# Optimization experiments

Measured on AMD Instinct MI355X. Metric: run time of the kernel, lower is better.

Reference implementation:

```python
import jax, jax.numpy as jnp
import numpy as np

D_MODEL = 1024
N_HEADS = 16
D_K = D_MODEL // N_HEADS


def setup_inputs() -> dict:
    key = jax.random.key(0)
    kx, kq, kk, kv, ko = jax.random.split(key, 5)
    s = 1.0 / np.sqrt(D_MODEL)
    return {
        "x": jax.random.normal(kx, (4, 2048, D_MODEL), dtype=jnp.float32),
        "W_q": jax.random.normal(kq, (D_MODEL, D_MODEL), dtype=jnp.float32) * s,
        "W_k": jax.random.normal(kk, (D_MODEL, D_MODEL), dtype=jnp.float32) * s,
        "W_v": jax.random.normal(kv, (D_MODEL, D_MODEL), dtype=jnp.float32) * s,
        "W_o": jax.random.normal(ko, (D_MODEL, D_MODEL), dtype=jnp.float32) * s,
    }


def reference(x, W_q, W_k, W_v, W_o):
    B, S, _ = x.shape
    # torch nn.Linear computes x @ W.T; our W_* stored as [out, in]-equivalent square,
    # use plain x @ W (equivalent parameterization for a random weight).
    def split_heads(t):  # [B,S,D] -> [B,H,S,d_k]
        return t.reshape(B, S, N_HEADS, D_K).transpose(0, 2, 1, 3)

    Q = split_heads(x @ W_q)
    K = split_heads(x @ W_k)
    V = split_heads(x @ W_v)
    scale = 1.0 / np.sqrt(D_K).astype(np.float32)
    scores = jnp.einsum('bhqd,bhkd->bhqk', Q, K) * scale  # [B,H,S,S]
    causal_mask = jnp.tril(jnp.ones((S, S), dtype=bool))  # True = keep
    scores = jnp.where(causal_mask, scores, jnp.float32(-jnp.inf))
    attn = jax.nn.softmax(scores, axis=-1)
    out = jnp.einsum('bhqk,bhkd->bhqd', attn, V)  # [B,H,S,d_k]
    out = out.transpose(0, 2, 1, 3).reshape(B, S, D_MODEL)
    return out @ W_o
```

## Files before the change

kernel.cpp:

```cpp
#include <hip/hip_runtime.h>
#include <hip/hip_bf16.h>
#include <stdint.h>

#define B_SZ 4
#define SEQ 2048
#define DM 1024
#define NH 16
#define DK 64
#define BH (B_SZ * NH)
#define M_TOT (B_SZ * SEQ)

typedef unsigned short u16;
typedef u16 u16x8 __attribute__((ext_vector_type(8)));
typedef __bf16 bf16x8 __attribute__((ext_vector_type(8)));
typedef float f32x4 __attribute__((ext_vector_type(4)));

__device__ __forceinline__ u16 f2bf(float f) {
    union { float f; uint32_t u; } v; v.f = f;
    uint32_t u = v.u;
    return (u16)((u + 0x7FFFu + ((u >> 16) & 1u)) >> 16);
}

__device__ __forceinline__ u16 f2bf_trunc(float f) {
    union { float f; uint32_t u; } v; v.f = f;
    return (u16)(v.u >> 16);
}

__device__ __forceinline__ f32x4 mfma16(u16x8 a, u16x8 b, f32x4 c) {
    return __builtin_amdgcn_mfma_f32_16x16x32_bf16(
        __builtin_bit_cast(bf16x8, a), __builtin_bit_cast(bf16x8, b), c, 0, 0, 0);
}

__device__ __forceinline__ void gload16_lds(const void* g, void* l) {
    __builtin_amdgcn_global_load_lds(
        (const __attribute__((address_space(1))) void*)(uintptr_t)g,
        (__attribute__((address_space(3))) void*)(uintptr_t)l, 16, 0, 0);
}

__global__ void cvt_bf16_kernel(const float* __restrict__ in, u16* __restrict__ out, int n4) {
    int i = blockIdx.x * blockDim.x + threadIdx.x;
    if (i < n4) {
        float4 v = ((const float4*)in)[i];
        ushort4 o;
        o.x = f2bf(v.x); o.y = f2bf(v.y); o.z = f2bf(v.z); o.w = f2bf(v.w);
        ((ushort4*)out)[i] = o;
    }
}

__global__ void transpose_w_kernel(const float* __restrict__ W0, const float* __restrict__ W1,
                                   u16* __restrict__ Wt) {
    __shared__ u16 tile[32][33];
    int bx = blockIdx.x, by = blockIdx.y, z = blockIdx.z;
    const float* W = z ? W1 : W0;
    u16* Wd = Wt + (size_t)z * DM * DM;
    int t = threadIdx.x;
    for (int i = 0; i < 4; i++) {
        int idx = t + i * 256;
        int r = idx >> 5, c = idx & 31;
        tile[r][c] = f2bf(W[(by * 32 + r) * DM + bx * 32 + c]);
    }
    __syncthreads();
    for (int i = 0; i < 4; i++) {
        int idx = t + i * 256;
        int r2 = idx >> 5, c2 = idx & 31;
        Wd[(bx * 32 + r2) * DM + by * 32 + c2] = tile[c2][r2];
    }
}

template <int AFP32, int MODE>
__global__ __launch_bounds__(256, 2) void gemm128(
    const void* __restrict__ Ain, const u16* __restrict__ Bt,
    void* __restrict__ C0p, void* __restrict__ C1p, float scale0) {
    __shared__ u16 As[128][32];
    __shared__ u16 Bs[128][32];
    const int K = DM;
    int m0 = blockIdx.x * 128;
    int n0 = blockIdx.y * 128;
    int tid = threadIdx.x;
    int lane = tid & 63, wave = tid >> 6;
    int quad = lane >> 4, l15 = lane & 15;
    int wm = wave >> 1, wn = wave & 1;

    f32x4 acc[4][4];
    for (int i = 0; i < 4; i++)
        for (int j = 0; j < 4; j++) acc[i][j] = f32x4{0.f, 0.f, 0.f, 0.f};

    int rS = lane >> 2;
    int cS = (lane & 3) * 8;

    for (int k0 = 0; k0 < K; k0 += 32) {
        __syncthreads();
        if (AFP32) {
            const float* A = (const float*)Ain;
            for (int i = 0; i < 4; i++) {
                int idx = tid + i * 256;
                int r = idx >> 3, c = (idx & 7) * 4;
                float4 v = *(const float4*)(&A[(size_t)(m0 + r) * K + k0 + c]);
                ushort4 o;
                o.x = f2bf(v.x); o.y = f2bf(v.y); o.z = f2bf(v.z); o.w = f2bf(v.w);
                *(ushort4*)(&As[r][c]) = o;
            }
        } else {
            const u16* A = (const u16*)Ain;
            const u16* ga = &A[(size_t)(m0 + wave * 32 + rS) * K + k0 + cS];
            gload16_lds(ga, &As[wave * 32][0]);
            gload16_lds(ga + (size_t)16 * K, &As[wave * 32 + 16][0]);
        }
        {
            const u16* gb = &Bt[(size_t)(n0 + wave * 32 + rS) * K + k0 + cS];
            gload16_lds(gb, &Bs[wave * 32][0]);
            gload16_lds(gb + (size_t)16 * K, &Bs[wave * 32 + 16][0]);
        }
        __syncthreads();
        u16x8 af[4], bfv[4];
        for (int mt = 0; mt < 4; mt++)
            af[mt] = *(const u16x8*)(&As[wm * 64 + mt * 16 + l15][quad * 8]);
        for (int nt = 0; nt < 4; nt++)
            bfv[nt] = *(const u16x8*)(&Bs[wn * 64 + nt * 16 + l15][quad * 8]);
        for (int mt = 0; mt < 4; mt++)
            for (int nt = 0; nt < 4; nt++)
                acc[mt][nt] = mfma16(af[mt], bfv[nt], acc[mt][nt]);
    }

    for (int mt = 0; mt < 4; mt++)
        for (int nt = 0; nt < 4; nt++)
            for (int r = 0; r < 4; r++) {
                int m = m0 + wm * 64 + mt * 16 + quad * 4 + r;
                int n = n0 + wn * 64 + nt * 16 + l15;
                float v = acc[mt][nt][r];
                if (MODE == 0) {
                    v *= (n < 1024) ? scale0 : 1.0f;
                    u16* C = (n < 1024) ? (u16*)C0p : (u16*)C1p;
                    int ne = n & 1023;
                    int b = m >> 11, s = m & 2047;
                    int h = ne >> 6, d = ne & 63;
                    C[(((size_t)(b * NH + h) * SEQ) + s) * DK + d] = f2bf(v);
                } else if (MODE == 1) {
                    ((float*)C0p)[(size_t)m * DM + n] = v;
                } else {
                    int b = m >> 11, s = m & 2047;
                    int h = n >> 6, d = n & 63;
                    ((u16*)C0p)[(((size_t)(b * NH + h) * DK) + d) * SEQ + s] = f2bf(v);
                }
            }
}

__global__ __launch_bounds__(256, 6) void attn_kernel(
    const u16* __restrict__ Qb, const u16* __restrict__ Kb,
    const u16* __restrict__ Vtb, u16* __restrict__ AOb) {
    __shared__ u16 Kl[2][64][32];
    __shared__ u16 Vl[2][64][32];
    __shared__ u16 Pl[64][68];

    int bh = blockIdx.x;
    int qs = 31 - blockIdx.y;
    int q0 = qs * 64;
    int tid = threadIdx.x, lane = tid & 63, wave = tid >> 6;
    int quad = lane >> 4, l15 = lane & 15;
    int b = bh >> 4, h = bh & 15;

    const u16* Qg = Qb + (size_t)bh * SEQ * DK;
    const u16* Kg = Kb + (size_t)bh * SEQ * DK;
    const u16* Vg = Vtb + (size_t)bh * DK * SEQ;

    int rS = lane >> 2;
    int cS = (lane & 3) * 8;
    u16* Pw = &Pl[wave * 16][0];

    u16x8 aq[2];
    for (int kc = 0; kc < 2; kc++)
        aq[kc] = *(const u16x8*)(
            &Qg[(size_t)(q0 + wave * 16 + l15) * DK + kc * 32 + quad * 8]);

    float lsum[4];
    f32x4 O[4];
    for (int r = 0; r < 4; r++) lsum[r] = 0.f;
    for (int nt = 0; nt < 4; nt++) O[nt] = f32x4{0.f, 0.f, 0.f, 0.f};

    for (int kt = 0; kt <= qs; kt++) {
        int k0 = kt * 64;
        __syncthreads();
        {
            const u16* gk = &Kg[(size_t)(k0 + wave * 16 + rS) * DK + cS];
            gload16_lds(gk, &Kl[0][wave * 16][0]);
            gload16_lds(gk + 32, &Kl[1][wave * 16][0]);
            const u16* gv = &Vg[(size_t)(wave * 16 + rS) * SEQ + k0 + cS];
            gload16_lds(gv, &Vl[0][wave * 16][0]);
            gload16_lds(gv + 32, &Vl[1][wave * 16][0]);
        }
        __syncthreads();

        f32x4 sc[4];
        for (int nt = 0; nt < 4; nt++) {
            u16x8 b0 = *(const u16x8*)(&Kl[0][nt * 16 + l15][quad * 8]);
            u16x8 b1 = *(const u16x8*)(&Kl[1][nt * 16 + l15][quad * 8]);
            f32x4 z = f32x4{0.f, 0.f, 0.f, 0.f};
            z = mfma16(aq[0], b0, z);
            z = mfma16(aq[1], b1, z);
            sc[nt] = z;
        }
        if (kt == qs) {
            for (int nt = 0; nt < 4; nt++)
                for (int r = 0; r < 4; r++) {
                    int qq = wave * 16 + quad * 4 + r;
                    int kk = nt * 16 + l15;
                    float e = exp2f(sc[nt][r]);
                    float pv = (kk <= qq) ? e : 0.f;
                    sc[nt][r] = pv;
                    lsum[r] += pv;
                }
        } else {
            for (int nt = 0; nt < 4; nt++)
                for (int r = 0; r < 4; r++) {
                    float pv = exp2f(sc[nt][r]);
                    sc[nt][r] = pv;
                    lsum[r] += pv;
                }
        }
        for (int nt = 0; nt < 4; nt++)
            for (int r = 0; r < 4; r++)
                Pw[(size_t)(quad * 4 + r) * 68 + nt * 16 + l15] = f2bf_trunc(sc[nt][r]);
        u16x8 ap0 = *(const u16x8*)(&Pw[(size_t)l15 * 68 + quad * 8]);
        u16x8 ap1 = *(const u16x8*)(&Pw[(size_t)l15 * 68 + 32 + quad * 8]);
        for (int nt = 0; nt < 4; nt++) {
            u16x8 b0 = *(const u16x8*)(&Vl[0][nt * 16 + l15][quad * 8]);
            u16x8 b1 = *(const u16x8*)(&Vl[1][nt * 16 + l15][quad * 8]);
            O[nt] = mfma16(ap0, b0, O[nt]);
            O[nt] = mfma16(ap1, b1, O[nt]);
        }
    }

    for (int r = 0; r < 4; r++) {
        float s = lsum[r];
        for (int off = 1; off < 16; off <<= 1) s += __shfl_xor(s, off, 64);
        float inv = 1.0f / s;
        int q = q0 + wave * 16 + quad * 4 + r;
        for (int nt = 0; nt < 4; nt++) {
            int d = nt * 16 + l15;
            AOb[((size_t)(b * SEQ + q)) * DM + h * DK + d] = f2bf(O[nt][r] * inv);
        }
    }
}

extern "C" void kernel_launch(void* const* d_in, const int* in_sizes, int n_in,
                              void* d_out, int out_size, void* d_ws, size_t ws_size,
                              hipStream_t stream) {
    const float* x = (const float*)d_in[0];
    const float* Wq = (const float*)d_in[1];
    const float* Wk = (const float*)d_in[2];
    const float* Wv = (const float*)d_in[3];
    const float* Wo = (const float*)d_in[4];
    float* out = (float*)d_out;

    const size_t HALF = (size_t)M_TOT * DM * 2;
    char* S0 = (char*)d_ws;
    char* S1 = (char*)d_ws + HALF;
    char* D0 = (char*)d_out;
    char* D1 = (char*)d_out + HALF;

    u16* xb  = (u16*)S0;
    u16* Qb  = (u16*)S1;
    u16* Kb  = (u16*)D1;
    u16* Vt  = (u16*)D0;
    u16* AOb = (u16*)S0;
    u16* wqk = (u16*)D0;
    u16* wvt = (u16*)S0;
    u16* wot = (u16*)S1;

    const float cscale = 0.125f * 1.44269504088896f;
    dim3 tg2(32, 32, 2);
    dim3 tg1(32, 32, 1);
    dim3 gg(M_TOT / 128, DM / 128);

    int n4 = M_TOT * DM / 4;
    cvt_bf16_kernel<<<n4 / 256, 256, 0, stream>>>(x, xb, n4);

    transpose_w_kernel<<<tg2, 256, 0, stream>>>(Wq, Wk, wqk);
    dim3 gqk(M_TOT / 128, 2048 / 128);
    gemm128<0, 0><<<gqk, 256, 0, stream>>>(xb, wqk, (void*)Qb, (void*)Kb, cscale);

    transpose_w_kernel<<<tg1, 256, 0, stream>>>(Wv, Wv, wvt);
    gemm128<1, 2><<<gg, 256, 0, stream>>>(x, wvt, (void*)Vt, (void*)Vt, 1.0f);

    dim3 ag(BH, 32);
    attn_kernel<<<ag, 256, 0, stream>>>(Qb, Kb, Vt, AOb);

    transpose_w_kernel<<<tg1, 256, 0, stream>>>(Wo, Wo, wot);
    gemm128<0, 1><<<gg, 256, 0, stream>>>(AOb, wot, (void*)out, (void*)out, 1.0f);
}
```

Measured before the change: 296.6 us.

## Restructure attention to per-wave paired query strips and widen GEMM K-tile

```diff
diff --git a/kernel.cpp b/kernel.cpp
--- a/kernel.cpp
+++ b/kernel.cpp
@@ -71,8 +71,8 @@
 __global__ __launch_bounds__(256, 2) void gemm128(
     const void* __restrict__ Ain, const u16* __restrict__ Bt,
     void* __restrict__ C0p, void* __restrict__ C1p, float scale0) {
-    __shared__ u16 As[128][32];
-    __shared__ u16 Bs[128][32];
+    __shared__ u16 As[128][64];
+    __shared__ u16 Bs[128][64];
     const int K = DM;
     int m0 = blockIdx.x * 128;
     int n0 = blockIdx.y * 128;
@@ -85,41 +85,47 @@
     for (int i = 0; i < 4; i++)
         for (int j = 0; j < 4; j++) acc[i][j] = f32x4{0.f, 0.f, 0.f, 0.f};
 
-    int rS = lane >> 2;
-    int cS = (lane & 3) * 8;
-
-    for (int k0 = 0; k0 < K; k0 += 32) {
+    int r8 = lane >> 3;
+    int c8 = (lane & 7) * 8;
+
+    for (int k0 = 0; k0 < K; k0 += 64) {
         __syncthreads();
         if (AFP32) {
             const float* A = (const float*)Ain;
-            for (int i = 0; i < 4; i++) {
-                int idx = tid + i * 256;
-                int r = idx >> 3, c = (idx & 7) * 4;
-                float4 v = *(const float4*)(&A[(size_t)(m0 + r) * K + k0 + c]);
-                ushort4 o;
-                o.x = f2bf(v.x); o.y = f2bf(v.y); o.z = f2bf(v.z); o.w = f2bf(v.w);
-                *(ushort4*)(&As[r][c]) = o;
+            for (int j = 0; j < 4; j++) {
+                int slot = tid + j * 256;
+                int r = slot >> 3, c = (slot & 7) * 8;
+                const float* g = &A[(size_t)(m0 + r) * K + k0 + c];
+                float4 v0 = *(const float4*)g;
+                float4 v1 = *(const float4*)(g + 4);
+                u16x8 o;
+                o[0] = f2bf(v0.x); o[1] = f2bf(v0.y); o[2] = f2bf(v0.z); o[3] = f2bf(v0.w);
+                o[4] = f2bf(v1.x); o[5] = f2bf(v1.y); o[6] = f2bf(v1.z); o[7] = f2bf(v1.w);
+                *(u16x8*)(&As[r][c]) = o;
             }
         } else {
             const u16* A = (const u16*)Ain;
-            const u16* ga = &A[(size_t)(m0 + wave * 32 + rS) * K + k0 + cS];
-            gload16_lds(ga, &As[wave * 32][0]);
-            gload16_lds(ga + (size_t)16 * K, &As[wave * 32 + 16][0]);
+            const u16* ga = &A[(size_t)(m0 + wave * 32 + r8) * K + k0 + c8];
+            for (int j = 0; j < 4; j++)
+                gload16_lds(ga + (size_t)(8 * j) * K, &As[wave * 32 + 8 * j][0]);
         }
         {
-            const u16* gb = &Bt[(size_t)(n0 + wave * 32 + rS) * K + k0 + cS];
-            gload16_lds(gb, &Bs[wave * 32][0]);
-            gload16_lds(gb + (size_t)16 * K, &Bs[wave * 32 + 16][0]);
+            const u16* gb = &Bt[(size_t)(n0 + wave * 32 + r8) * K + k0 + c8];
+            for (int j = 0; j < 4; j++)
+                gload16_lds(gb + (size_t)(8 * j) * K, &Bs[wave * 32 + 8 * j][0]);
         }
         __syncthreads();
-        u16x8 af[4], bfv[4];
+        u16x8 af[4][2], bfv[4][2];
         for (int mt = 0; mt < 4; mt++)
-            af[mt] = *(const u16x8*)(&As[wm * 64 + mt * 16 + l15][quad * 8]);
+            for (int kc = 0; kc < 2; kc++)
+                af[mt][kc] = *(const u16x8*)(&As[wm * 64 + mt * 16 + l15][kc * 32 + quad * 8]);
         for (int nt = 0; nt < 4; nt++)
-            bfv[nt] = *(const u16x8*)(&Bs[wn * 64 + nt * 16 + l15][quad * 8]);
-        for (int mt = 0; mt < 4; mt++)
-            for (int nt = 0; nt < 4; nt++)
-                acc[mt][nt] = mfma16(af[mt], bfv[nt], acc[mt][nt]);
+            for (int kc = 0; kc < 2; kc++)
+                bfv[nt][kc] = *(const u16x8*)(&Bs[wn * 64 + nt * 16 + l15][kc * 32 + quad * 8]);
+        for (int kc = 0; kc < 2; kc++)
+            for (int mt = 0; mt < 4; mt++)
+                for (int nt = 0; nt < 4; nt++)
+                    acc[mt][nt] = mfma16(af[mt][kc], bfv[nt][kc], acc[mt][nt]);
     }
 
     for (int mt = 0; mt < 4; mt++)
@@ -145,16 +151,13 @@
             }
 }
 
-__global__ __launch_bounds__(256, 6) void attn_kernel(
+__global__ __launch_bounds__(256, 4) void attn_kernel(
     const u16* __restrict__ Qb, const u16* __restrict__ Kb,
     const u16* __restrict__ Vtb, u16* __restrict__ AOb) {
-    __shared__ u16 Kl[2][64][32];
-    __shared__ u16 Vl[2][64][32];
-    __shared__ u16 Pl[64][68];
+    __shared__ u16 Pl[4][32][68];
 
     int bh = blockIdx.x;
-    int qs = 31 - blockIdx.y;
-    int q0 = qs * 64;
+    int yy = blockIdx.y;
     int tid = threadIdx.x, lane = tid & 63, wave = tid >> 6;
     int quad = lane >> 4, l15 = lane & 15;
     int b = bh >> 4, h = bh & 15;
@@ -162,83 +165,92 @@
     const u16* Qg = Qb + (size_t)bh * SEQ * DK;
     const u16* Kg = Kb + (size_t)bh * SEQ * DK;
     const u16* Vg = Vtb + (size_t)bh * DK * SEQ;
-
-    int rS = lane >> 2;
-    int cS = (lane & 3) * 8;
-    u16* Pw = &Pl[wave * 16][0];
-
-    u16x8 aq[2];
-    for (int kc = 0; kc < 2; kc++)
-        aq[kc] = *(const u16x8*)(
-            &Qg[(size_t)(q0 + wave * 16 + l15) * DK + kc * 32 + quad * 8]);
-
-    float lsum[4];
-    f32x4 O[4];
-    for (int r = 0; r < 4; r++) lsum[r] = 0.f;
-    for (int nt = 0; nt < 4; nt++) O[nt] = f32x4{0.f, 0.f, 0.f, 0.f};
-
-    for (int kt = 0; kt <= qs; kt++) {
-        int k0 = kt * 64;
-        __syncthreads();
-        {
-            const u16* gk = &Kg[(size_t)(k0 + wave * 16 + rS) * DK + cS];
-            gload16_lds(gk, &Kl[0][wave * 16][0]);
-            gload16_lds(gk + 32, &Kl[1][wave * 16][0]);
-            const u16* gv = &Vg[(size_t)(wave * 16 + rS) * SEQ + k0 + cS];
-            gload16_lds(gv, &Vl[0][wave * 16][0]);
-            gload16_lds(gv + 32, &Vl[1][wave * 16][0]);
-        }
-        __syncthreads();
-
-        f32x4 sc[4];
-        for (int nt = 0; nt < 4; nt++) {
-            u16x8 b0 = *(const u16x8*)(&Kl[0][nt * 16 + l15][quad * 8]);
-            u16x8 b1 = *(const u16x8*)(&Kl[1][nt * 16 + l15][quad * 8]);
-            f32x4 z = f32x4{0.f, 0.f, 0.f, 0.f};
-            z = mfma16(aq[0], b0, z);
-            z = mfma16(aq[1], b1, z);
-            sc[nt] = z;
-        }
-        if (kt == qs) {
+    u16* Pw = &Pl[wave][0][0];
+
+    for (int ph = 0; ph < 2; ph++) {
+        int s0 = yy * 4 + wave;
+        int strip = ph ? (63 - s0) : s0;
+        int q0 = strip * 32;
+        int lastkt = strip >> 1;
+
+        u16x8 aq[2][2];
+        for (int m = 0; m < 2; m++)
+            for (int kc = 0; kc < 2; kc++)
+                aq[m][kc] = *(const u16x8*)(
+                    &Qg[(size_t)(q0 + m * 16 + l15) * DK + kc * 32 + quad * 8]);
+
+        float lsum[2][4];
+        f32x4 O[2][4];
+        for (int m = 0; m < 2; m++)
+            for (int r = 0; r < 4; r++) lsum[m][r] = 0.f;
+        for (int m = 0; m < 2; m++)
+            for (int nt = 0; nt < 4; nt++) O[m][nt] = f32x4{0.f, 0.f, 0.f, 0.f};
+
+        for (int kt = 0; kt <= lastkt; kt++) {
+            int k0 = kt * 64;
+            bool masked = (kt == lastkt);
+
+            u16x8 kf[4][2];
             for (int nt = 0; nt < 4; nt++)
-                for (int r = 0; r < 4; r++) {
-                    int qq = wave * 16 + quad * 4 + r;
-                    int kk = nt * 16 + l15;
-                    float e = exp2f(sc[nt][r]);
-                    float pv = (kk <= qq) ? e : 0.f;
-                    sc[nt][r] = pv;
-                    lsum[r] += pv;
+                for (int kc = 0; kc < 2; kc++)
+                    kf[nt][kc] = *(const u16x8*)(
+                        &Kg[(size_t)(k0 + nt * 16 + l15) * DK + kc * 32 + quad * 8]);
+
+            for (int nt = 0; nt < 4; nt++) {
+                for (int m = 0; m < 2; m++) {
+                    f32x4 z = f32x4{0.f, 0.f, 0.f, 0.f};
+                    z = mfma16(aq[m][0], kf[nt][0], z);
+                    z = mfma16(aq[m][1], kf[nt][1], z);
+                    if (masked) {
+                        for (int r = 0; r < 4; r++) {
+                            int qa = q0 + m * 16 + quad * 4 + r;
+                            int ka = k0 + nt * 16 + l15;
+                            float pv = (ka <= qa) ? exp2f(z[r]) : 0.f;
+                            lsum[m][r] += pv;
+                            Pw[(size_t)(m * 16 + quad * 4 + r) * 68 + nt * 16 + l15] =
+                                f2bf_trunc(pv);
+                        }
+                    } else {
+                        for (int r = 0; r < 4; r++) {
+                            float pv = exp2f(z[r]);
+                            lsum[m][r] += pv;
+                            Pw[(size_t)(m * 16 + quad * 4 + r) * 68 + nt * 16 + l15] =
+                                f2bf_trunc(pv);
+                        }
+                    }
                 }
-        } else {
+            }
+
+            u16x8 vf[4][2];
             for (int nt = 0; nt < 4; nt++)
-                for (int r = 0; r < 4; r++) {
-                    float pv = exp2f(sc[nt][r]);
-                    sc[nt][r] = pv;
-                    lsum[r] += pv;
+                for (int kc = 0; kc < 2; kc++)
+                    vf[nt][kc] = *(const u16x8*)(
+                        &Vg[(size_t)(nt * 16 + l15) * SEQ + k0 + kc * 32 + quad * 8]);
+
+            u16x8 ap[2][2];
+            for (int m = 0; m < 2; m++)
+                for (int kc = 0; kc < 2; kc++)
+                    ap[m][kc] = *(const u16x8*)(
+                        &Pw[(size_t)(m * 16 + l15) * 68 + kc * 32 + quad * 8]);
+
+            for (int nt = 0; nt < 4; nt++)
+                for (int m = 0; m < 2; m++) {
+                    O[m][nt] = mfma16(ap[m][0], vf[nt][0], O[m][nt]);
+                    O[m][nt] = mfma16(ap[m][1], vf[nt][1], O[m][nt]);
                 }
         }
-        for (int nt = 0; nt < 4; nt++)
-            for (int r = 0; r < 4; r++)
-                Pw[(size_t)(quad * 4 + r) * 68 + nt * 16 + l15] = f2bf_trunc(sc[nt][r]);
-        u16x8 ap0 = *(const u16x8*)(&Pw[(size_t)l15 * 68 + quad * 8]);
-        u16x8 ap1 = *(const u16x8*)(&Pw[(size_t)l15 * 68 + 32 + quad * 8]);
-        for (int nt = 0; nt < 4; nt++) {
-            u16x8 b0 = *(const u16x8*)(&Vl[0][nt * 16 + l15][quad * 8]);
-            u16x8 b1 = *(const u16x8*)(&Vl[1][nt * 16 + l15][quad * 8]);
-            O[nt] = mfma16(ap0, b0, O[nt]);
-            O[nt] = mfma16(ap1, b1, O[nt]);
-        }
-    }
-
-    for (int r = 0; r < 4; r++) {
-        float s = lsum[r];
-        for (int off = 1; off < 16; off <<= 1) s += __shfl_xor(s, off, 64);
-        float inv = 1.0f / s;
-        int q = q0 + wave * 16 + quad * 4 + r;
-        for (int nt = 0; nt < 4; nt++) {
-            int d = nt * 16 + l15;
-            AOb[((size_t)(b * SEQ + q)) * DM + h * DK + d] = f2bf(O[nt][r] * inv);
-        }
+
+        for (int m = 0; m < 2; m++)
+            for (int r = 0; r < 4; r++) {
+                float s = lsum[m][r];
+                for (int off = 1; off < 16; off <<= 1) s += __shfl_xor(s, off, 64);
+                float inv = 1.0f / s;
+                int q = q0 + m * 16 + quad * 4 + r;
+                for (int nt = 0; nt < 4; nt++) {
+                    int d = nt * 16 + l15;
+                    AOb[((size_t)(b * SEQ + q)) * DM + h * DK + d] = f2bf(O[m][nt][r] * inv);
+                }
+            }
     }
 }
 
@@ -282,7 +294,7 @@
     transpose_w_kernel<<<tg1, 256, 0, stream>>>(Wv, Wv, wvt);
     gemm128<1, 2><<<gg, 256, 0, stream>>>(x, wvt, (void*)Vt, (void*)Vt, 1.0f);
 
-    dim3 ag(BH, 32);
+    dim3 ag(BH, 16);
     attn_kernel<<<ag, 256, 0, stream>>>(Qb, Kb, Vt, AOb);
 
     transpose_w_kernel<<<tg1, 256, 0, stream>>>(Wo, Wo, wot);
```

Result: slower. 452.9 us (+52.7%).
